# Kernel tuning notes

Hardware: AMD Instinct MI355X
Metric: run time of the kernel (lower is better)

## Reference

```python
import jax, jax.numpy as jnp
import numpy as np

B, C, H, W = 8, 256, 64, 64
HEADS, H_SP, W_SP = 8, 64, 4  # idx=0: H_sp=resolution[0], W_sp=split_size
D = C // HEADS
SCALE = D ** -0.5
HH, WW = H // H_SP, W // W_SP  # 1, 16 (no padding needed)


def setup_inputs() -> dict:
    key = jax.random.key(0)
    k1, k2, k3 = jax.random.split(key, 3)
    temp = jax.random.normal(k1, (B, 3, C, H, W), dtype=jnp.float32)
    get_v_weight = jax.random.normal(k2, (C, 1, 3, 3), dtype=jnp.float32) * 0.1
    get_v_bias = jax.random.normal(k3, (C,), dtype=jnp.float32) * 0.1
    return {"temp": temp, "get_v_weight": get_v_weight, "get_v_bias": get_v_bias}


def _im2win_shuffle(x):
    # x: (B, C, H, W); H split as (H_SP, HH) with H_SP OUTER (shuffled windows)
    x = x.reshape(B, HEADS, D, H_SP, HH, W_SP, WW)
    x = x.transpose(0, 4, 6, 1, 3, 5, 2)  # b hh ww h H_sp W_sp d
    return x.reshape(B * HH * WW, HEADS, H_SP * W_SP, D)


def reference(temp, get_v_weight, get_v_bias):
    # H, W are multiples of H_SP, W_SP -> pad is zero (faithful to F.pad path)
    q, k, v = temp[:, 0], temp[:, 1], temp[:, 2]
    qw = _im2win_shuffle(q) * SCALE
    kw = _im2win_shuffle(k)
    vw = _im2win_shuffle(v)

    # LePE: depthwise 3x3 conv applied per shuffled window
    vimg = v.reshape(B, C, H_SP, HH, W_SP, WW).transpose(0, 3, 5, 1, 2, 4)
    vimg = vimg.reshape(B * HH * WW, C, H_SP, W_SP)
    lepe = jax.lax.conv_general_dilated(
        vimg, get_v_weight, (1, 1), ((1, 1), (1, 1)),
        dimension_numbers=("NCHW", "OIHW", "NCHW"), feature_group_count=C,
    ) + get_v_bias[None, :, None, None]
    lepe = lepe.reshape(B * HH * WW, HEADS, D, H_SP * W_SP).transpose(0, 1, 3, 2)

    attn = jax.nn.softmax(jnp.einsum("whqd,whkd->whqk", qw, kw), axis=-1)
    x = jnp.einsum("whqk,whkd->whqd", attn, vw) + lepe  # (nW, h, S, d)

    # windows2img_shuffle -> (B, C, H, W), then raw .view to (B, H, W, C)
    x = x.reshape(B, HH, WW, HEADS, H_SP, W_SP, D)
    x = x.transpose(0, 3, 6, 4, 1, 5, 2).reshape(B, C, H, W)
    x = x.reshape(B, H, W, C)  # raw memory view, matches torch .view
    return x.reshape(B, H * W, C)
```

## Files before the change

### kernel.cpp

```cpp
#include <hip/hip_runtime.h>


typedef __attribute__((ext_vector_type(8))) short bf16x8;
typedef __attribute__((ext_vector_type(4))) float floatx4;
typedef unsigned short ushort_t;
typedef unsigned int uint_t;

constexpr float QSCALE = 0.25503486f;

__device__ __forceinline__ ushort_t f2bf(float f) {
    union { float f; uint_t u; } v; v.f = f;
    uint_t r = v.u + 0x7fffu + ((v.u >> 16) & 1u);
    return (ushort_t)(r >> 16);
}
__device__ __forceinline__ float bf2f(ushort_t h) {
    union { uint_t u; float f; } v; v.u = ((uint_t)h) << 16;
    return v.f;
}
__device__ __forceinline__ int swzrow(int r) {
    return (r & 56) | ((r ^ (r >> 2)) & 7);
}

constexpr int TSTR  = 1288;
constexpr int VBASE = 16 * TSTR;
constexpr int VSTR  = 1288;
constexpr int PBASE = VBASE + 16 * VSTR;
constexpr int SMU   = PBASE + 16 * 512;
constexpr int LSTR  = 2568;
constexpr int OSTR  = 1058;

__global__ __launch_bounds__(1024, 4)
void fused_kernel(const float* __restrict__ temp, const float* __restrict__ wgt,
                  const float* __restrict__ bias, float* __restrict__ out)
{
    const int bid = blockIdx.x;
    const int hd = bid & 7;
    const int qq = (bid >> 3) & 3;
    const int b  = bid >> 5;

    __shared__ __align__(16) ushort_t SM[SMU];

    const int u = threadIdx.x;
    const int w8 = u >> 6;
    const int ln = u & 63;
    const int lm = ln & 15, q4 = ln >> 4, l7 = ln & 7, b8 = (ln >> 3) & 1;

    const float4* Tq4 = (const float4*)temp + ((size_t)((b * 3 + 0) * 256 + hd * 32)) * 1024;
    const float4* Tk4 = Tq4 + (size_t)256 * 1024;
    const float4* Tv4 = Tk4 + (size_t)256 * 1024;

    union F4 { float4 v; float a[4]; };

    int paw0[4], paw1[4];
    #pragma unroll
    for (int r = 0; r < 4; r++) {
        paw0[r] = PBASE + w8 * 512 + swzrow(b8 * 16 + q4 * 4 + r) * 8 + l7;
        paw1[r] = PBASE + w8 * 512 + swzrow((2 + b8) * 16 + q4 * 4 + r) * 8 + l7;
    }
    const int pard = PBASE + w8 * 512 + swzrow(ln) * 8;

    bf16x8 qa[4];
    #pragma unroll
    for (int pass = 0; pass < 2; pass++) {
        const int hb = qq * 16 + pass * 8;
        #pragma unroll
        for (int i = 0; i < 4; i++) {
            const int flat = i * 1024 + u;
            const int w4 = flat & 15, h8 = (flat >> 4) & 7, d = flat >> 7;
            F4 v; v.v = Tq4[(size_t)d * 1024 + (hb + h8) * 16 + w4];
            const int tl = h8 * 4 + (w4 >> 2);
            const int wb = (w4 & 3) * 4;
            #pragma unroll
            for (int j = 0; j < 4; j++)
                SM[(wb + j) * TSTR + tl * 40 + d] = f2bf(v.a[j] * QSCALE);
        }
        __syncthreads();
        #pragma unroll
        for (int Tl = 0; Tl < 2; Tl++)
            qa[pass * 2 + Tl] = *(const bf16x8*)&SM[w8 * TSTR + (Tl * 16 + lm) * 40 + q4 * 8];
        __syncthreads();
    }

    floatx4 acc[4][2];
    float lrow[4][4];
    #pragma unroll
    for (int T = 0; T < 4; T++) {
        acc[T][0] = (floatx4)0.0f; acc[T][1] = (floatx4)0.0f;
        #pragma unroll
        for (int r = 0; r < 4; r++) lrow[T][r] = 0.0f;
    }

    for (int kt = 0; kt < 8; kt++) {
        #pragma unroll
        for (int i = 0; i < 4; i++) {
            const int flat = i * 1024 + u;
            const int w4 = flat & 15, h8 = (flat >> 4) & 7, d = flat >> 7;
            F4 v; v.v = Tk4[(size_t)d * 1024 + (kt * 8 + h8) * 16 + w4];
            const int tl = h8 * 4 + (w4 >> 2);
            const int wb = (w4 & 3) * 4;
            #pragma unroll
            for (int j = 0; j < 4; j++)
                SM[(wb + j) * TSTR + tl * 40 + d] = f2bf(v.a[j]);
        }
        #pragma unroll
        for (int i = 0; i < 4; i++) {
            const int flat = i * 1024 + u;
            const int w4 = flat & 15, h8 = (flat >> 4) & 7, d = flat >> 7;
            F4 v; v.v = Tv4[(size_t)d * 1024 + (kt * 8 + h8) * 16 + w4];
            const int tl = h8 * 4 + (w4 >> 2);
            const int wb = (w4 & 3) * 4;
            #pragma unroll
            for (int j = 0; j < 4; j++)
                SM[VBASE + (wb + j) * VSTR + d * 40 + tl] = f2bf(v.a[j]);
        }
        __syncthreads();

        const bf16x8 kb0 = *(const bf16x8*)&SM[w8 * TSTR + lm * 40 + q4 * 8];
        const bf16x8 kb1 = *(const bf16x8*)&SM[w8 * TSTR + (16 + lm) * 40 + q4 * 8];
        const bf16x8 vb0 = *(const bf16x8*)&SM[VBASE + w8 * VSTR + lm * 40 + q4 * 8];
        const bf16x8 vb1 = *(const bf16x8*)&SM[VBASE + w8 * VSTR + (16 + lm) * 40 + q4 * 8];
        #pragma unroll
        for (int T = 0; T < 4; T++) {
            floatx4 s0 = __builtin_amdgcn_mfma_f32_16x16x32_bf16(qa[T], kb0, (floatx4)0.0f, 0, 0, 0);
            floatx4 s1 = __builtin_amdgcn_mfma_f32_16x16x32_bf16(qa[T], kb1, (floatx4)0.0f, 0, 0, 0);
            #pragma unroll
            for (int r = 0; r < 4; r++) {
                const float p0 = exp2f(s0[r]);
                const float p1 = exp2f(s1[r]);
                const ushort_t h0 = f2bf(p0), h1 = f2bf(p1);
                lrow[T][r] += bf2f(h0) + bf2f(h1);
                SM[paw0[r]] = h0;
                SM[paw1[r]] = h1;
            }
            const bf16x8 pa = *(const bf16x8*)&SM[pard];
            acc[T][0] = __builtin_amdgcn_mfma_f32_16x16x32_bf16(pa, vb0, acc[T][0], 0, 0, 0);
            acc[T][1] = __builtin_amdgcn_mfma_f32_16x16x32_bf16(pa, vb1, acc[T][1], 0, 0, 0);
        }
        __syncthreads();
    }

    #pragma unroll
    for (int i = 0; i < 9; i++) {
        const int flat = i * 1024 + u;
        const int f4w = flat & 15, rowid = flat >> 4;
        const int d = rowid / 18, hl = rowid - d * 18;
        const int hh = qq * 16 - 1 + hl;
        F4 v;
        if ((unsigned)hh < 64u) v.v = Tv4[(size_t)d * 1024 + hh * 16 + f4w];
        else { v.a[0] = 0.f; v.a[1] = 0.f; v.a[2] = 0.f; v.a[3] = 0.f; }
        const int cx = f4w >> 2, wb = (f4w & 3) * 4;
        #pragma unroll
        for (int j = 0; j < 4; j++)
            SM[(wb + j) * LSTR + d * 80 + hl * 4 + cx] = f2bf(v.a[j]);
    }
    __syncthreads();

    float wc[2][9], bs2[2];
    #pragma unroll
    for (int dt = 0; dt < 2; dt++) {
        const int d = dt * 16 + lm;
        #pragma unroll
        for (int k = 0; k < 9; k++) wc[dt][k] = wgt[(hd * 32 + d) * 9 + k];
        bs2[dt] = bias[hd * 32 + d];
    }

    #pragma unroll
    for (int T = 0; T < 4; T++) {
        float inv[4];
        #pragma unroll
        for (int r = 0; r < 4; r++) {
            float ls = lrow[T][r];
            ls += __shfl_xor(ls, 1); ls += __shfl_xor(ls, 2);
            ls += __shfl_xor(ls, 4); ls += __shfl_xor(ls, 8);
            inv[r] = 1.0f / ls;
        }
        #pragma unroll
        for (int dt = 0; dt < 2; dt++) {
            const int d = dt * 16 + lm;
            float vv[3][4];
            #pragma unroll
            for (int dy = 0; dy < 3; dy++) {
                const int hl = T * 4 + q4 + dy;
                #pragma unroll
                for (int cx = 0; cx < 4; cx++)
                    vv[dy][cx] = bf2f(SM[w8 * LSTR + d * 80 + hl * 4 + cx]);
            }
            #pragma unroll
            for (int r = 0; r < 4; r++) {
                float lep = bs2[dt];
                #pragma unroll
                for (int dy = 0; dy < 3; dy++) {
                    #pragma unroll
                    for (int kx = 0; kx < 3; kx++) {
                        const int wsrc = r + kx - 1;
                        if (wsrc >= 0 && wsrc < 4) lep += wc[dt][dy * 3 + kx] * vv[dy][wsrc];
                    }
                }
                acc[T][dt][r] = acc[T][dt][r] * inv[r] + lep;
            }
        }
    }
    __syncthreads();

    float* Ob = (float*)SM;
    float4* out4 = (float4*)out + ((size_t)(b * 256 + hd * 32)) * 1024;
    #pragma unroll
    for (int half = 0; half < 2; half++) {
        #pragma unroll
        for (int Tl = 0; Tl < 2; Tl++) {
            const int T = half * 2 + Tl;
            #pragma unroll
            for (int dt = 0; dt < 2; dt++) {
                #pragma unroll
                for (int r = 0; r < 4; r++)
                    Ob[w8 * OSTR + (Tl * 16 + q4 * 4 + r) * 33 + dt * 16 + lm] = acc[T][dt][r];
            }
        }
        __syncthreads();
        #pragma unroll
        for (int i = 0; i < 4; i++) {
            const int flat = i * 1024 + u;
            const int f4 = flat & 3, ql = (flat >> 2) & 31, dd = flat >> 7;
            float4 o;
            o.x = Ob[(f4 * 4 + 0) * OSTR + ql * 33 + dd];
            o.y = Ob[(f4 * 4 + 1) * OSTR + ql * 33 + dd];
            o.z = Ob[(f4 * 4 + 2) * OSTR + ql * 33 + dd];
            o.w = Ob[(f4 * 4 + 3) * OSTR + ql * 33 + dd];
            out4[(size_t)dd * 1024 + (qq * 64 + half * 32 + ql) * 4 + f4] = o;
        }
        __syncthreads();
    }
}

extern "C" void kernel_launch(void* const* d_in, const int* in_sizes, int n_in,
                              void* d_out, int out_size, void* d_ws, size_t ws_size,
                              hipStream_t stream) {
    const float* temp = (const float*)d_in[0];
    const float* wgt  = (const float*)d_in[1];
    const float* bias = (const float*)d_in[2];
    float* out = (float*)d_out;
    (void)d_ws; (void)ws_size;
    fused_kernel<<<dim3(256), dim3(1024), 0, stream>>>(temp, wgt, bias, out);
}
```

Baseline: 225.4 us.

## Keep softmax probabilities in registers by transposing S MFMA operands

The QK^T MFMA now takes K as the A operand and Q as B, so each lane's score outputs already sit in the layout the PV MFMA needs as its A operand. This removes the LDS round-trip for P, along with its scratch region and swizzle. The row-sum becomes a per-lane partial reduced with cross-lane shuffles. Staging of Q, K and V is reworked to use packed bf16 conversion (v_cvt_pk_bf16_f32) with 64-bit LDS stores. Smaller strides shrink shared memory, and the launch bound changes to request 8 waves per EU.

After: 239.0 us. 1.06x slower.

```diff
diff --git a/kernel.cpp b/kernel.cpp
--- a/kernel.cpp
+++ b/kernel.cpp
@@ -17,19 +17,49 @@
     union { uint_t u; float f; } v; v.u = ((uint_t)h) << 16;
     return v.f;
 }
-__device__ __forceinline__ int swzrow(int r) {
-    return (r & 56) | ((r ^ (r >> 2)) & 7);
-}
-
-constexpr int TSTR  = 1288;
-constexpr int VBASE = 16 * TSTR;
-constexpr int VSTR  = 1288;
-constexpr int PBASE = VBASE + 16 * VSTR;
-constexpr int SMU   = PBASE + 16 * 512;
-constexpr int LSTR  = 2568;
+__device__ __forceinline__ float bfu2f(uint_t bits) {
+    union { uint_t u; float f; } v; v.u = bits; return v.f;
+}
+__device__ __forceinline__ uint_t cvtpk(float lo, float hi) {
+    uint_t r;
+    asm("v_cvt_pk_bf16_f32 %0, %1, %2" : "=v"(r) : "v"(lo), "v"(hi));
+    return r;
+}
+
+constexpr int KP    = 1280;
+constexpr int VBASE = 16 * KP;
+constexpr int VP    = 1280;
+constexpr int SMU   = VBASE + 16 * VP;
+constexpr int LSTR  = 2432;
 constexpr int OSTR  = 1058;
 
-__global__ __launch_bounds__(1024, 4)
+template<bool SCALE>
+__device__ __forceinline__ void stage_kq(const float4* __restrict__ src,
+                                         ushort_t* dst, int u, int hb) {
+    const int w4 = u & 15, h8 = (u >> 4) & 7, d = (u >> 7) * 4;
+    union F4 { float4 v; float a[4]; } v0, v1, v2, v3;
+    const size_t base = (size_t)(hb + h8) * 16 + w4;
+    v0.v = src[(size_t)(d + 0) * 1024 + base];
+    v1.v = src[(size_t)(d + 1) * 1024 + base];
+    v2.v = src[(size_t)(d + 2) * 1024 + base];
+    v3.v = src[(size_t)(d + 3) * 1024 + base];
+    const int tl = h8 * 4 + (w4 >> 2), a = w4 & 3;
+    #pragma unroll
+    for (int j = 0; j < 4; j++) {
+        uint_t lo, hi;
+        if (SCALE) {
+            lo = cvtpk(v0.a[j] * QSCALE, v1.a[j] * QSCALE);
+            hi = cvtpk(v2.a[j] * QSCALE, v3.a[j] * QSCALE);
+        } else {
+            lo = cvtpk(v0.a[j], v1.a[j]);
+            hi = cvtpk(v2.a[j], v3.a[j]);
+        }
+        uint2 pk; pk.x = lo; pk.y = hi;
+        *(uint2*)&dst[(a * 4 + j) * KP + tl * 40 + d] = pk;
+    }
+}
+
+__global__ __launch_bounds__(1024) __attribute__((amdgpu_waves_per_eu(8)))
 void fused_kernel(const float* __restrict__ temp, const float* __restrict__ wgt,
                   const float* __restrict__ bias, float* __restrict__ out)
 {
@@ -43,98 +73,72 @@
     const int u = threadIdx.x;
     const int w8 = u >> 6;
     const int ln = u & 63;
-    const int lm = ln & 15, q4 = ln >> 4, l7 = ln & 7, b8 = (ln >> 3) & 1;
+    const int lm = ln & 15, q4 = ln >> 4;
 
     const float4* Tq4 = (const float4*)temp + ((size_t)((b * 3 + 0) * 256 + hd * 32)) * 1024;
     const float4* Tk4 = Tq4 + (size_t)256 * 1024;
     const float4* Tv4 = Tk4 + (size_t)256 * 1024;
 
-    union F4 { float4 v; float a[4]; };
-
-    int paw0[4], paw1[4];
-    #pragma unroll
-    for (int r = 0; r < 4; r++) {
-        paw0[r] = PBASE + w8 * 512 + swzrow(b8 * 16 + q4 * 4 + r) * 8 + l7;
-        paw1[r] = PBASE + w8 * 512 + swzrow((2 + b8) * 16 + q4 * 4 + r) * 8 + l7;
-    }
-    const int pard = PBASE + w8 * 512 + swzrow(ln) * 8;
-
     bf16x8 qa[4];
     #pragma unroll
     for (int pass = 0; pass < 2; pass++) {
-        const int hb = qq * 16 + pass * 8;
-        #pragma unroll
-        for (int i = 0; i < 4; i++) {
-            const int flat = i * 1024 + u;
-            const int w4 = flat & 15, h8 = (flat >> 4) & 7, d = flat >> 7;
-            F4 v; v.v = Tq4[(size_t)d * 1024 + (hb + h8) * 16 + w4];
-            const int tl = h8 * 4 + (w4 >> 2);
-            const int wb = (w4 & 3) * 4;
-            #pragma unroll
-            for (int j = 0; j < 4; j++)
-                SM[(wb + j) * TSTR + tl * 40 + d] = f2bf(v.a[j] * QSCALE);
-        }
+        stage_kq<true>(Tq4, SM, u, qq * 16 + pass * 8);
         __syncthreads();
         #pragma unroll
         for (int Tl = 0; Tl < 2; Tl++)
-            qa[pass * 2 + Tl] = *(const bf16x8*)&SM[w8 * TSTR + (Tl * 16 + lm) * 40 + q4 * 8];
+            qa[pass * 2 + Tl] = *(const bf16x8*)&SM[w8 * KP + (Tl * 16 + lm) * 40 + q4 * 8];
         __syncthreads();
     }
 
     floatx4 acc[4][2];
-    float lrow[4][4];
+    float lsum[4];
     #pragma unroll
     for (int T = 0; T < 4; T++) {
         acc[T][0] = (floatx4)0.0f; acc[T][1] = (floatx4)0.0f;
-        #pragma unroll
-        for (int r = 0; r < 4; r++) lrow[T][r] = 0.0f;
-    }
+        lsum[T] = 0.0f;
+    }
+
+    const int k0row = ((lm >> 2) << 3) + (lm & 3);
+    const int pKb = w8 * KP;
+    const int pVb = VBASE + w8 * VP;
 
     for (int kt = 0; kt < 8; kt++) {
-        #pragma unroll
-        for (int i = 0; i < 4; i++) {
-            const int flat = i * 1024 + u;
-            const int w4 = flat & 15, h8 = (flat >> 4) & 7, d = flat >> 7;
-            F4 v; v.v = Tk4[(size_t)d * 1024 + (kt * 8 + h8) * 16 + w4];
-            const int tl = h8 * 4 + (w4 >> 2);
-            const int wb = (w4 & 3) * 4;
-            #pragma unroll
-            for (int j = 0; j < 4; j++)
-                SM[(wb + j) * TSTR + tl * 40 + d] = f2bf(v.a[j]);
-        }
-        #pragma unroll
-        for (int i = 0; i < 4; i++) {
-            const int flat = i * 1024 + u;
-            const int w4 = flat & 15, h8 = (flat >> 4) & 7, d = flat >> 7;
-            F4 v; v.v = Tv4[(size_t)d * 1024 + (kt * 8 + h8) * 16 + w4];
-            const int tl = h8 * 4 + (w4 >> 2);
-            const int wb = (w4 & 3) * 4;
-            #pragma unroll
-            for (int j = 0; j < 4; j++)
-                SM[VBASE + (wb + j) * VSTR + d * 40 + tl] = f2bf(v.a[j]);
-        }
-        __syncthreads();
-
-        const bf16x8 kb0 = *(const bf16x8*)&SM[w8 * TSTR + lm * 40 + q4 * 8];
-        const bf16x8 kb1 = *(const bf16x8*)&SM[w8 * TSTR + (16 + lm) * 40 + q4 * 8];
-        const bf16x8 vb0 = *(const bf16x8*)&SM[VBASE + w8 * VSTR + lm * 40 + q4 * 8];
-        const bf16x8 vb1 = *(const bf16x8*)&SM[VBASE + w8 * VSTR + (16 + lm) * 40 + q4 * 8];
+        stage_kq<false>(Tk4, SM, u, kt * 8);
+        {
+            const int a = u & 3, h8 = (u >> 2) & 7, dv = u >> 5;
+            union F4 { float4 v; float a[4]; } w0, w1, w2, w3;
+            const size_t vb = (size_t)dv * 1024 + (size_t)(kt * 8 + h8) * 16 + a;
+            w0.v = Tv4[vb];  w1.v = Tv4[vb + 4];  w2.v = Tv4[vb + 8];  w3.v = Tv4[vb + 12];
+            #pragma unroll
+            for (int j = 0; j < 4; j++) {
+                uint2 pk;
+                pk.x = cvtpk(w0.a[j], w1.a[j]);
+                pk.y = cvtpk(w2.a[j], w3.a[j]);
+                *(uint2*)&SM[VBASE + (a * 4 + j) * VP + dv * 40 + h8 * 4] = pk;
+            }
+        }
+        __syncthreads();
+
+        const bf16x8 kb0 = *(const bf16x8*)&SM[pKb + k0row * 40 + q4 * 8];
+        const bf16x8 kb1 = *(const bf16x8*)&SM[pKb + (k0row + 4) * 40 + q4 * 8];
+        const bf16x8 vb0 = *(const bf16x8*)&SM[pVb + lm * 40 + q4 * 8];
+        const bf16x8 vb1 = *(const bf16x8*)&SM[pVb + (16 + lm) * 40 + q4 * 8];
         #pragma unroll
         for (int T = 0; T < 4; T++) {
-            floatx4 s0 = __builtin_amdgcn_mfma_f32_16x16x32_bf16(qa[T], kb0, (floatx4)0.0f, 0, 0, 0);
-            floatx4 s1 = __builtin_amdgcn_mfma_f32_16x16x32_bf16(qa[T], kb1, (floatx4)0.0f, 0, 0, 0);
-            #pragma unroll
-            for (int r = 0; r < 4; r++) {
-                const float p0 = exp2f(s0[r]);
-                const float p1 = exp2f(s1[r]);
-                const ushort_t h0 = f2bf(p0), h1 = f2bf(p1);
-                lrow[T][r] += bf2f(h0) + bf2f(h1);
-                SM[paw0[r]] = h0;
-                SM[paw1[r]] = h1;
-            }
-            const bf16x8 pa = *(const bf16x8*)&SM[pard];
-            acc[T][0] = __builtin_amdgcn_mfma_f32_16x16x32_bf16(pa, vb0, acc[T][0], 0, 0, 0);
-            acc[T][1] = __builtin_amdgcn_mfma_f32_16x16x32_bf16(pa, vb1, acc[T][1], 0, 0, 0);
+            floatx4 s0 = __builtin_amdgcn_mfma_f32_16x16x32_bf16(kb0, qa[T], (floatx4)0.0f, 0, 0, 0);
+            floatx4 s1 = __builtin_amdgcn_mfma_f32_16x16x32_bf16(kb1, qa[T], (floatx4)0.0f, 0, 0, 0);
+            const uint_t u0 = cvtpk(exp2f(s0[0]), exp2f(s0[1]));
+            const uint_t u1 = cvtpk(exp2f(s0[2]), exp2f(s0[3]));
+            const uint_t u2 = cvtpk(exp2f(s1[0]), exp2f(s1[1]));
+            const uint_t u3 = cvtpk(exp2f(s1[2]), exp2f(s1[3]));
+            lsum[T] += bfu2f(u0 << 16) + bfu2f(u0 & 0xffff0000u)
+                     + bfu2f(u1 << 16) + bfu2f(u1 & 0xffff0000u)
+                     + bfu2f(u2 << 16) + bfu2f(u2 & 0xffff0000u)
+                     + bfu2f(u3 << 16) + bfu2f(u3 & 0xffff0000u);
+            union { uint_t w[4]; bf16x8 v; } pa;
+            pa.w[0] = u0; pa.w[1] = u1; pa.w[2] = u2; pa.w[3] = u3;
+            acc[T][0] = __builtin_amdgcn_mfma_f32_16x16x32_bf16(pa.v, vb0, acc[T][0], 0, 0, 0);
+            acc[T][1] = __builtin_amdgcn_mfma_f32_16x16x32_bf16(pa.v, vb1, acc[T][1], 0, 0, 0);
         }
         __syncthreads();
     }
@@ -145,13 +149,13 @@
         const int f4w = flat & 15, rowid = flat >> 4;
         const int d = rowid / 18, hl = rowid - d * 18;
         const int hh = qq * 16 - 1 + hl;
-        F4 v;
+        union F4 { float4 v; float a[4]; } v;
         if ((unsigned)hh < 64u) v.v = Tv4[(size_t)d * 1024 + hh * 16 + f4w];
         else { v.a[0] = 0.f; v.a[1] = 0.f; v.a[2] = 0.f; v.a[3] = 0.f; }
         const int cx = f4w >> 2, wb = (f4w & 3) * 4;
         #pragma unroll
         for (int j = 0; j < 4; j++)
-            SM[(wb + j) * LSTR + d * 80 + hl * 4 + cx] = f2bf(v.a[j]);
+            SM[(wb + j) * LSTR + d * 76 + hl * 4 + cx] = f2bf(v.a[j]);
     }
     __syncthreads();
 
@@ -166,14 +170,13 @@
 
     #pragma unroll
     for (int T = 0; T < 4; T++) {
+        float tot = lsum[T];
+        tot += __shfl_xor(tot, 16);
+        tot += __shfl_xor(tot, 32);
         float inv[4];
         #pragma unroll
-        for (int r = 0; r < 4; r++) {
-            float ls = lrow[T][r];
-            ls += __shfl_xor(ls, 1); ls += __shfl_xor(ls, 2);
-            ls += __shfl_xor(ls, 4); ls += __shfl_xor(ls, 8);
-            inv[r] = 1.0f / ls;
-        }
+        for (int r = 0; r < 4; r++) inv[r] = 1.0f / __shfl(tot, q4 * 4 + r);
+
         #pragma unroll
         for (int dt = 0; dt < 2; dt++) {
             const int d = dt * 16 + lm;
@@ -183,7 +186,7 @@
                 const int hl = T * 4 + q4 + dy;
                 #pragma unroll
                 for (int cx = 0; cx < 4; cx++)
-                    vv[dy][cx] = bf2f(SM[w8 * LSTR + d * 80 + hl * 4 + cx]);
+                    vv[dy][cx] = bf2f(SM[w8 * LSTR + d * 76 + hl * 4 + cx]);
             }
             #pragma unroll
             for (int r = 0; r < 4; r++) {
```
